# Kernel optimization log

Hardware: AMD Instinct MI355X
Metric: run time of the kernel (lower is better)

## Reference

```python
import jax, jax.numpy as jnp
import numpy as np

B, T, E, H = 2, 2048, 1024, 16
S = E // H
LN_EPS = 1e-5


def _layer_norm(x, w, b):
    # normalize over last axis (head dim s)
    mu = jnp.mean(x, axis=-1, keepdims=True)
    var = jnp.mean(jnp.square(x - mu), axis=-1, keepdims=True)
    return (x - mu) * jax.lax.rsqrt(var + LN_EPS) * w + b


def setup_inputs() -> dict:
    key = jax.random.key(0)
    ks = jax.random.split(key, 7)
    scale = 0.02
    return {
        "queries": jax.random.normal(ks[0], (B, T, E), dtype=jnp.float32),
        "keys": jax.random.normal(ks[1], (B, T, E), dtype=jnp.float32),
        "values": jax.random.normal(ks[2], (B, T, E), dtype=jnp.float32),
        "Wq": jax.random.normal(ks[3], (E, E), dtype=jnp.float32) * scale,
        "Wk": jax.random.normal(ks[4], (E, E), dtype=jnp.float32) * scale,
        "Wv": jax.random.normal(ks[5], (E, E), dtype=jnp.float32) * scale,
        "Wo": jax.random.normal(ks[6], (E, E), dtype=jnp.float32) * scale,
        "bo": jnp.zeros((E,), dtype=jnp.float32),
        "q_ln_w": jnp.ones((S,), dtype=jnp.float32),
        "q_ln_b": jnp.zeros((S,), dtype=jnp.float32),
        "k_ln_w": jnp.ones((S,), dtype=jnp.float32),
        "k_ln_b": jnp.zeros((S,), dtype=jnp.float32),
    }


def reference(queries, keys, values, Wq, Wk, Wv, Wo, bo, q_ln_w, q_ln_b, k_ln_w, k_ln_b):
    b, tq, e = queries.shape
    tk = keys.shape[1]
    h, s = H, S

    q = (queries @ Wq).reshape(b, tq, h, s)
    k = (keys @ Wk).reshape(b, tk, h, s)
    v = (values @ Wv).reshape(b, tk, h, s)

    # kqnorm: per-head LayerNorm over s
    q = _layer_norm(q, q_ln_w, q_ln_b)
    k = _layer_norm(k, k_ln_w, k_ln_b)

    # NOTE: original scales q and k each by emb**(-1/4) (NOT head_dim)
    inv4 = jnp.asarray(e, q.dtype) ** -0.25
    q = q * inv4
    k = k * inv4

    dot = jnp.einsum("bqhs,bkhs->bhqk", q, k)  # [b,h,tq,tk]

    # causal mask (mask_diagonal=False -> keep diagonal): mask j > i
    causal = jnp.tril(jnp.ones((tq, tk), dtype=bool))
    dot = jnp.where(causal, dot, jnp.asarray(-jnp.inf, dot.dtype))

    attn = jax.nn.softmax(dot, axis=-1)

    out = jnp.einsum("bhqk,bkhs->bqhs", attn, v).reshape(b, tq, e)
    return out @ Wo + bo
```

## Files before the change

kernel.cpp:

```cpp
#include <hip/hip_runtime.h>

#define Tdim 2048
#define Edim 1024
#define Hdim 16
#define Sdim 64
#define Mdim 4096
#define LN_EPS 1e-5f
#define QKSCALE 0.21233045007200477f

typedef __bf16 bf16x8 __attribute__((ext_vector_type(8)));
typedef float f32x4 __attribute__((ext_vector_type(4)));

__device__ __forceinline__ unsigned short f2bf(float f) {
  union { float f; unsigned int u; } c; c.f = f;
  unsigned int u = c.u;
  return (unsigned short)((u + 0x7FFFu + ((u >> 16) & 1u)) >> 16);
}

__device__ __forceinline__ float exp2fast(float x) {
  float r;
  asm("v_exp_f32 %0, %1" : "=v"(r) : "v"(x));
  return r;
}

__device__ __forceinline__ void gl_lds16(const void* g, void* l) {
  __builtin_amdgcn_global_load_lds(
      (const __attribute__((address_space(1))) void*)g,
      (__attribute__((address_space(3))) void*)l, 16, 0, 0);
}

__device__ __forceinline__ unsigned int pk2bf(unsigned int lo, unsigned int hi) {
  return __builtin_amdgcn_perm(hi, lo, 0x07060302u);
}

__global__ __launch_bounds__(256) void prep_k(
    const float* __restrict__ X0, const float* __restrict__ X1, const float* __restrict__ X2,
    unsigned short* __restrict__ Y0, unsigned short* __restrict__ Y1,
    unsigned short* __restrict__ Y2,
    const float* __restrict__ W0, const float* __restrict__ W1,
    const float* __restrict__ W2, const float* __restrict__ W3,
    unsigned short* __restrict__ O0, unsigned short* __restrict__ O1,
    unsigned short* __restrict__ O2, unsigned short* __restrict__ O3) {
  int bid = blockIdx.x, tid = threadIdx.x;
  if (bid < 6144) {
    int zi = bid >> 11, blk = bid & 2047;
    const float* X = zi == 0 ? X0 : zi == 1 ? X1 : X2;
    unsigned short* Y = zi == 0 ? Y0 : zi == 1 ? Y1 : Y2;
    size_t i = ((size_t)blk * 256 + tid) * 8;
    uint4 a = *(const uint4*)&X[i];
    uint4 b = *(const uint4*)&X[i + 4];
    uint4 o;
    o.x = pk2bf(a.x, a.y);
    o.y = pk2bf(a.z, a.w);
    o.z = pk2bf(b.x, b.y);
    o.w = pk2bf(b.z, b.w);
    *(uint4*)&Y[i] = o;
  } else {
    int wb = bid - 6144;
    int zi = wb >> 10, tile = wb & 1023;
    const float* W = zi == 0 ? W0 : zi == 1 ? W1 : zi == 2 ? W2 : W3;
    unsigned short* O = zi == 0 ? O0 : zi == 1 ? O1 : zi == 2 ? O2 : O3;
    __shared__ float t[32][33];
    int n0 = (tile & 31) * 32, k0 = (tile >> 5) * 32;
    int tx = tid & 31, ty = tid >> 5;
    for (int yy = ty; yy < 32; yy += 8)
      t[yy][tx] = W[(size_t)(k0 + yy) * Edim + n0 + tx];
    __syncthreads();
    for (int yy = ty; yy < 32; yy += 8)
      O[(size_t)(n0 + yy) * Edim + k0 + tx] = f2bf(t[tx][yy]);
  }
}

__global__ __launch_bounds__(256, 4) void qkv_k(
    const unsigned short* __restrict__ Qa, const unsigned short* __restrict__ Ka,
    const unsigned short* __restrict__ Va,
    const unsigned short* __restrict__ Bq, const unsigned short* __restrict__ Bk,
    const unsigned short* __restrict__ Bv,
    const float* __restrict__ qlnw, const float* __restrict__ qlnb,
    const float* __restrict__ klnw, const float* __restrict__ klnb,
    unsigned short* __restrict__ Oq, unsigned short* __restrict__ Ok,
    unsigned short* __restrict__ Ov) {
  __shared__ unsigned short As[128 * 32];
  __shared__ unsigned short Bs[128 * 32];
  int f = blockIdx.x;
  int L = (f & 7) * 96 + (f >> 3);
  int bx = L & 7, by = (L >> 3) & 31, z = L >> 8;
  const unsigned short* A = z == 0 ? Qa : z == 1 ? Ka : Va;
  const unsigned short* Bt = z == 0 ? Bq : z == 1 ? Bk : Bv;
  const float* lnw = z == 0 ? qlnw : klnw;
  const float* lnb = z == 0 ? qlnb : klnb;
  unsigned short* obf = z == 0 ? Oq : z == 1 ? Ok : Ov;

  int tid = threadIdx.x, lane = tid & 63, w = tid >> 6;
  int wr = w >> 1, wc = w & 1;
  int lg = lane >> 4, l15 = lane & 15;
  int cr = lane >> 2, sl = lane & 3;
  int m0 = by * 128, n0 = bx * 128;

  f32x4 acc[4][4];
#pragma unroll
  for (int i = 0; i < 4; ++i)
#pragma unroll
    for (int j = 0; j < 4; ++j) acc[i][j] = f32x4{0.f, 0.f, 0.f, 0.f};

  for (int ks = 0; ks < 32; ++ks) {
    int k0 = ks * 32;
    __syncthreads();
#pragma unroll
    for (int q = 0; q < 2; ++q) {
      int c = w * 2 + q, r = c * 16 + cr;
      gl_lds16(&A[(size_t)(m0 + r) * Edim + k0 + ((sl ^ (r & 3)) * 8)], &As[c * 512]);
    }
#pragma unroll
    for (int q = 0; q < 2; ++q) {
      int c = w * 2 + q, r = c * 16 + cr;
      gl_lds16(&Bt[(size_t)(n0 + r) * Edim + k0 + ((sl ^ (r & 3)) * 8)], &Bs[c * 512]);
    }
    __syncthreads();
    const unsigned short* pA = (z == 2) ? &Bs[0] : &As[0];
    const unsigned short* pB = (z == 2) ? &As[0] : &Bs[0];
    bf16x8 a[4], bb[4];
#pragma unroll
    for (int i = 0; i < 4; ++i) {
      int r = wr * 64 + i * 16 + l15;
      a[i] = *(const bf16x8*)&pA[r * 32 + ((lg ^ (r & 3)) * 8)];
    }
#pragma unroll
    for (int j = 0; j < 4; ++j) {
      int r = wc * 64 + j * 16 + l15;
      bb[j] = *(const bf16x8*)&pB[r * 32 + ((lg ^ (r & 3)) * 8)];
    }
    __builtin_amdgcn_s_setprio(1);
#pragma unroll
    for (int i = 0; i < 4; ++i)
#pragma unroll
      for (int j = 0; j < 4; ++j)
        acc[i][j] = __builtin_amdgcn_mfma_f32_16x16x32_bf16(a[i], bb[j], acc[i][j], 0, 0, 0);
    __builtin_amdgcn_s_setprio(0);
  }

  if (z < 2) {
    int mb = m0 + wr * 64;
    int h = (n0 >> 6) + wc;
#pragma unroll
    for (int i = 0; i < 4; ++i) {
#pragma unroll
      for (int r = 0; r < 4; ++r) {
        float xv[4];
#pragma unroll
        for (int j = 0; j < 4; ++j) xv[j] = acc[i][j][r];
        float sum = xv[0] + xv[1] + xv[2] + xv[3];
        float sq = xv[0] * xv[0] + xv[1] * xv[1] + xv[2] * xv[2] + xv[3] * xv[3];
#pragma unroll
        for (int off = 1; off < 16; off <<= 1) {
          sum += __shfl_xor(sum, off);
          sq += __shfl_xor(sq, off);
        }
        float mean = sum * (1.f / 64.f);
        float var = sq * (1.f / 64.f) - mean * mean;
        float rstd = rsqrtf(var + LN_EPS);
        int m = mb + i * 16 + (lg << 2) + r;
        int bb2 = m >> 11, tt = m & 2047;
        size_t base = ((size_t)(bb2 * Hdim + h) * Tdim + tt) * Sdim;
#pragma unroll
        for (int j = 0; j < 4; ++j) {
          int s = j * 16 + l15;
          float ov = ((xv[j] - mean) * rstd * lnw[s] + lnb[s]) * QKSCALE;
          obf[base + s] = f2bf(ov);
        }
      }
    }
  } else {
#pragma unroll
    for (int i = 0; i < 4; ++i)
#pragma unroll
      for (int r = 0; r < 4; ++r) {
        int hc = n0 + wr * 64 + i * 16 + (lg << 2) + r;
        int h = hc >> 6, s = hc & 63;
#pragma unroll
        for (int j = 0; j < 4; ++j) {
          int tk = m0 + wc * 64 + j * 16 + l15;
          int bb2 = tk >> 11, tt = tk & 2047;
          obf[(((size_t)(bb2 * Hdim + h) * Sdim + s)) * Tdim + tt] = f2bf(acc[i][j][r]);
        }
      }
  }
}

__global__ __launch_bounds__(256, 4) void gemmo_k(
    const unsigned short* __restrict__ A, const unsigned short* __restrict__ Bt,
    const float* __restrict__ bias, float* __restrict__ ofp) {
  __shared__ unsigned short As[128 * 32];
  __shared__ unsigned short Bs[64 * 32];
  int f = blockIdx.x;
  int L = (f & 7) * 64 + (f >> 3);
  int bx = L & 15, by = L >> 4;
  int tid = threadIdx.x, lane = tid & 63, w = tid >> 6;
  int wr = w >> 1, wc = w & 1;
  int lg = lane >> 4, l15 = lane & 15;
  int cr = lane >> 2, sl = lane & 3;
  int m0 = by * 128, n0 = bx * 64;

  f32x4 acc[4][2];
#pragma unroll
  for (int i = 0; i < 4; ++i)
#pragma unroll
    for (int j = 0; j < 2; ++j) acc[i][j] = f32x4{0.f, 0.f, 0.f, 0.f};

  for (int ks = 0; ks < 32; ++ks) {
    int k0 = ks * 32;
    __syncthreads();
#pragma unroll
    for (int q = 0; q < 2; ++q) {
      int c = w * 2 + q, r = c * 16 + cr;
      gl_lds16(&A[(size_t)(m0 + r) * Edim + k0 + ((sl ^ (r & 3)) * 8)], &As[c * 512]);
    }
    {
      int c = w, r = c * 16 + cr;
      gl_lds16(&Bt[(size_t)(n0 + r) * Edim + k0 + ((sl ^ (r & 3)) * 8)], &Bs[c * 512]);
    }
    __syncthreads();
    bf16x8 a[4], bb[2];
#pragma unroll
    for (int i = 0; i < 4; ++i) {
      int r = wr * 64 + i * 16 + l15;
      a[i] = *(const bf16x8*)&As[r * 32 + ((lg ^ (r & 3)) * 8)];
    }
#pragma unroll
    for (int j = 0; j < 2; ++j) {
      int r = wc * 32 + j * 16 + l15;
      bb[j] = *(const bf16x8*)&Bs[r * 32 + ((lg ^ (r & 3)) * 8)];
    }
    __builtin_amdgcn_s_setprio(1);
#pragma unroll
    for (int i = 0; i < 4; ++i)
#pragma unroll
      for (int j = 0; j < 2; ++j)
        acc[i][j] = __builtin_amdgcn_mfma_f32_16x16x32_bf16(a[i], bb[j], acc[i][j], 0, 0, 0);
    __builtin_amdgcn_s_setprio(0);
  }

  int mb = m0 + wr * 64, nb = n0 + wc * 32;
#pragma unroll
  for (int i = 0; i < 4; ++i)
#pragma unroll
    for (int r = 0; r < 4; ++r) {
      int m = mb + i * 16 + (lg << 2) + r;
#pragma unroll
      for (int j = 0; j < 2; ++j) {
        int n = nb + j * 16 + l15;
        ofp[(size_t)m * Edim + n] = acc[i][j][r] + bias[n];
      }
    }
}

__global__ __launch_bounds__(256) void flash_k(
    const unsigned short* __restrict__ Qn, const unsigned short* __restrict__ Kn,
    const unsigned short* __restrict__ Vb, unsigned short* __restrict__ Ob) {
  __shared__ unsigned short Qs[4096];
  __shared__ unsigned short Ks[2][4096];
  __shared__ unsigned short Vt[2][4096];
  __shared__ unsigned short Ps[4][1024];

  int wid0 = blockIdx.x;
  int idx = wid0 >> 3;
  int bh = (wid0 & 7) * 4 + (idx & 3);
  int qseg = 31 - (idx >> 2);
  int nt = qseg + 1;

  int tid = threadIdx.x, lane = tid & 63, w = tid >> 6;
  int lg = lane >> 4, l15 = lane & 15;
  int lr = lane >> 3, ls = lane & 7;
  const unsigned short* Qg = Qn + ((size_t)bh * Tdim + (size_t)qseg * 64) * Sdim;
  const unsigned short* Kg = Kn + (size_t)bh * Tdim * Sdim;
  const unsigned short* Vg = Vb + (size_t)bh * Sdim * Tdim;
  int b = bh >> 4, h = bh & 15;

  auto stageK = [&](int tt, int kb) {
    const unsigned short* src = Kg + (size_t)tt * 64 * 64;
#pragma unroll
    for (int q = 0; q < 2; ++q) {
      int c = w * 2 + q, r = c * 8 + lr;
      gl_lds16(&src[r * 64 + ((ls ^ (r & 7)) * 8)], &Ks[kb][c * 512]);
    }
  };
  auto stageV = [&](int tt, int vb) {
    const unsigned short* src = Vg + tt * 64;
#pragma unroll
    for (int q = 0; q < 2; ++q) {
      int c = w * 2 + q, r = c * 8 + lr;
      gl_lds16(&src[(size_t)r * Tdim + ((ls ^ (r & 7)) * 8)], &Vt[vb][c * 512]);
    }
  };

#pragma unroll
  for (int q = 0; q < 2; ++q) {
    int c = w * 2 + q, r = c * 8 + lr;
    gl_lds16(&Qg[r * 64 + ((ls ^ (r & 7)) * 8)], &Qs[c * 512]);
  }
  stageK(0, 0);
  stageV(0, 0);

  float mrun = -1e30f;
  float lrun[4] = {0.f, 0.f, 0.f, 0.f};
  f32x4 o[4];
#pragma unroll
  for (int js = 0; js < 4; ++js) o[js] = f32x4{0.f, 0.f, 0.f, 0.f};

  __syncthreads();

  bf16x8 aq[2];
  {
    int rq = w * 16 + l15;
    aq[0] = *(const bf16x8*)&Qs[rq * 64 + ((lg ^ (rq & 7)) * 8)];
    aq[1] = *(const bf16x8*)&Qs[rq * 64 + (((4 + lg) ^ (rq & 7)) * 8)];
  }

  for (int t = 0; t < nt; ++t) {
    int cur = t & 1;
    if (t + 1 < nt) {
      stageK(t + 1, cur ^ 1);
      stageV(t + 1, cur ^ 1);
    }
    f32x4 sf[4];
#pragma unroll
    for (int j = 0; j < 4; ++j) sf[j] = f32x4{0.f, 0.f, 0.f, 0.f};
    const unsigned short* Kc = &Ks[cur][0];
    __builtin_amdgcn_s_setprio(1);
#pragma unroll
    for (int kx = 0; kx < 2; ++kx) {
#pragma unroll
      for (int j = 0; j < 4; ++j) {
        int rk = j * 16 + l15;
        bf16x8 bk = *(const bf16x8*)&Kc[rk * 64 + (((kx * 4 + lg) ^ (rk & 7)) * 8)];
        sf[j] = __builtin_amdgcn_mfma_f32_16x16x32_bf16(aq[kx], bk, sf[j], 0, 0, 0);
      }
    }
    __builtin_amdgcn_s_setprio(0);
    if (t == qseg) {
#pragma unroll
      for (int j = 0; j < 4; ++j)
#pragma unroll
        for (int rr = 0; rr < 4; ++rr)
          if (j * 16 + l15 > w * 16 + (lg << 2) + rr) sf[j][rr] = -1e30f;
    }
    float mx = -3e38f;
#pragma unroll
    for (int j = 0; j < 4; ++j)
#pragma unroll
      for (int rr = 0; rr < 4; ++rr) mx = fmaxf(mx, sf[j][rr]);
#pragma unroll
    for (int off = 1; off < 16; off <<= 1) mx = fmaxf(mx, __shfl_xor(mx, off));
    if (__any(mx > mrun + 8.f)) {
      float mnew = fmaxf(mrun, mx);
      float alpha = exp2fast(mrun - mnew);
      mrun = mnew;
#pragma unroll
      for (int rr = 0; rr < 4; ++rr) lrun[rr] *= alpha;
#pragma unroll
      for (int js = 0; js < 4; ++js) o[js] *= alpha;
    }
    unsigned short* Pw = &Ps[w][0];
#pragma unroll
    for (int j = 0; j < 4; ++j) {
      int og = 2 * j + (l15 >> 3);
#pragma unroll
      for (int rr = 0; rr < 4; ++rr) {
        float p = exp2fast(sf[j][rr] - mrun);
        lrun[rr] += p;
        union { float f; unsigned int u; } cu;
        cu.f = p;
        int qr = (lg << 2) + rr;
        Pw[qr * 64 + ((og ^ (qr & 7)) * 8) + (l15 & 7)] = (unsigned short)(cu.u >> 16);
      }
    }
    const unsigned short* Vc = &Vt[cur][0];
    __builtin_amdgcn_s_setprio(1);
#pragma unroll
    for (int kx = 0; kx < 2; ++kx) {
      bf16x8 ap = *(const bf16x8*)&Pw[l15 * 64 + (((kx * 4 + lg) ^ (l15 & 7)) * 8)];
#pragma unroll
      for (int js = 0; js < 4; ++js) {
        int rv = js * 16 + l15;
        bf16x8 bv = *(const bf16x8*)&Vc[rv * 64 + (((kx * 4 + lg) ^ (rv & 7)) * 8)];
        o[js] = __builtin_amdgcn_mfma_f32_16x16x32_bf16(ap, bv, o[js], 0, 0, 0);
      }
    }
    __builtin_amdgcn_s_setprio(0);
    __syncthreads();
  }

#pragma unroll
  for (int rr = 0; rr < 4; ++rr) {
    float l = lrun[rr];
#pragma unroll
    for (int off = 1; off < 16; off <<= 1) l += __shfl_xor(l, off);
    float inv = 1.f / l;
    int tg = qseg * 64 + w * 16 + (lg << 2) + rr;
    size_t base = ((size_t)b * Tdim + tg) * Edim + h * 64;
#pragma unroll
    for (int js = 0; js < 4; ++js) Ob[base + js * 16 + l15] = f2bf(o[js][rr] * inv);
  }
}

extern "C" void kernel_launch(void* const* d_in, const int* in_sizes, int n_in,
                              void* d_out, int out_size, void* d_ws, size_t ws_size,
                              hipStream_t stream) {
  const float* queries = (const float*)d_in[0];
  const float* keys    = (const float*)d_in[1];
  const float* values  = (const float*)d_in[2];
  const float* Wq = (const float*)d_in[3];
  const float* Wk = (const float*)d_in[4];
  const float* Wv = (const float*)d_in[5];
  const float* Wo = (const float*)d_in[6];
  const float* bo = (const float*)d_in[7];
  const float* qlnw = (const float*)d_in[8];
  const float* qlnb = (const float*)d_in[9];
  const float* klnw = (const float*)d_in[10];
  const float* klnb = (const float*)d_in[11];
  float* out = (float*)d_out;

  unsigned short* Wtq = (unsigned short*)d_ws;
  unsigned short* Wtk = Wtq + 1024 * 1024;
  unsigned short* Wtv = Wtk + 1024 * 1024;
  unsigned short* Wto = Wtv + 1024 * 1024;
  unsigned short* Qn  = Wto + 1024 * 1024;
  unsigned short* Kn  = Qn + (size_t)Mdim * Edim;
  unsigned short* Vb  = Kn + (size_t)Mdim * Edim;
  unsigned short* Qa  = Vb + (size_t)Mdim * Edim;
  unsigned short* Ka  = Qa + (size_t)Mdim * Edim;
  unsigned short* Va  = Ka + (size_t)Mdim * Edim;
  unsigned short* Ob  = Qa;

  prep_k<<<10240, 256, 0, stream>>>(queries, keys, values, Qa, Ka, Va,
                                    Wq, Wk, Wv, Wo, Wtq, Wtk, Wtv, Wto);
  qkv_k<<<768, 256, 0, stream>>>(Qa, Ka, Va, Wtq, Wtk, Wtv,
                                 qlnw, qlnb, klnw, klnb, Qn, Kn, Vb);
  flash_k<<<1024, 256, 0, stream>>>(Qn, Kn, Vb, Ob);
  gemmo_k<<<512, 256, 0, stream>>>(Ob, Wto, bo, out);
}
```

Before: 220.7 us.

## Transpose QK^T MFMA so each lane owns one query row in softmax

Swaps the MFMA operands for the score tile so the result is S^T, with each lane's 16 values belonging to a single query row. Row max and row sum now need only two cross-lane shuffles instead of four per reduction, and P is packed two-at-a-time into bf16 and written with 8-byte LDS stores instead of 16 scalar 2-byte stores. Rescaling O and the final normalization need per-row alpha and 1/l broadcast by shuffle, which adds a few shuffles on the rare rescale path and in the epilogue.

```diff
diff --git a/kernel.cpp b/kernel.cpp
--- a/kernel.cpp
+++ b/kernel.cpp
@@ -302,7 +302,7 @@
   stageV(0, 0);
 
   float mrun = -1e30f;
-  float lrun[4] = {0.f, 0.f, 0.f, 0.f};
+  float lrun = 0.f;
   f32x4 o[4];
 #pragma unroll
   for (int js = 0; js < 4; ++js) o[js] = f32x4{0.f, 0.f, 0.f, 0.f};
@@ -315,6 +315,7 @@
     aq[0] = *(const bf16x8*)&Qs[rq * 64 + ((lg ^ (rq & 7)) * 8)];
     aq[1] = *(const bf16x8*)&Qs[rq * 64 + (((4 + lg) ^ (rq & 7)) * 8)];
   }
+  unsigned int swz = (unsigned)(l15 & 7) << 4;
 
   for (int t = 0; t < nt; ++t) {
     int cur = t & 1;
@@ -332,8 +333,8 @@
 #pragma unroll
       for (int j = 0; j < 4; ++j) {
         int rk = j * 16 + l15;
-        bf16x8 bk = *(const bf16x8*)&Kc[rk * 64 + (((kx * 4 + lg) ^ (rk & 7)) * 8)];
-        sf[j] = __builtin_amdgcn_mfma_f32_16x16x32_bf16(aq[kx], bk, sf[j], 0, 0, 0);
+        bf16x8 ak = *(const bf16x8*)&Kc[rk * 64 + (((kx * 4 + lg) ^ (rk & 7)) * 8)];
+        sf[j] = __builtin_amdgcn_mfma_f32_16x16x32_bf16(ak, aq[kx], sf[j], 0, 0, 0);
       }
     }
     __builtin_amdgcn_s_setprio(0);
@@ -342,43 +343,47 @@
       for (int j = 0; j < 4; ++j)
 #pragma unroll
         for (int rr = 0; rr < 4; ++rr)
-          if (j * 16 + l15 > w * 16 + (lg << 2) + rr) sf[j][rr] = -1e30f;
-    }
-    float mx = -3e38f;
-#pragma unroll
-    for (int j = 0; j < 4; ++j)
-#pragma unroll
-      for (int rr = 0; rr < 4; ++rr) mx = fmaxf(mx, sf[j][rr]);
-#pragma unroll
-    for (int off = 1; off < 16; off <<= 1) mx = fmaxf(mx, __shfl_xor(mx, off));
+          if (j * 16 + (lg << 2) + rr > w * 16 + l15) sf[j][rr] = -1e30f;
+    }
+    float mx = fmaxf(fmaxf(fmaxf(sf[0][0], sf[0][1]), fmaxf(sf[0][2], sf[0][3])),
+                     fmaxf(fmaxf(sf[1][0], sf[1][1]), fmaxf(sf[1][2], sf[1][3])));
+    mx = fmaxf(mx, fmaxf(fmaxf(fmaxf(sf[2][0], sf[2][1]), fmaxf(sf[2][2], sf[2][3])),
+                         fmaxf(fmaxf(sf[3][0], sf[3][1]), fmaxf(sf[3][2], sf[3][3]))));
+    mx = fmaxf(mx, __shfl_xor(mx, 16));
+    mx = fmaxf(mx, __shfl_xor(mx, 32));
     if (__any(mx > mrun + 8.f)) {
       float mnew = fmaxf(mrun, mx);
       float alpha = exp2fast(mrun - mnew);
       mrun = mnew;
-#pragma unroll
-      for (int rr = 0; rr < 4; ++rr) lrun[rr] *= alpha;
-#pragma unroll
-      for (int js = 0; js < 4; ++js) o[js] *= alpha;
+      lrun *= alpha;
+      float ar[4];
+#pragma unroll
+      for (int rr = 0; rr < 4; ++rr)
+        ar[rr] = __shfl(alpha, (lg << 4) | ((lg << 2) + rr));
+#pragma unroll
+      for (int js = 0; js < 4; ++js)
+#pragma unroll
+        for (int rr = 0; rr < 4; ++rr) o[js][rr] *= ar[rr];
     }
     unsigned short* Pw = &Ps[w][0];
 #pragma unroll
     for (int j = 0; j < 4; ++j) {
-      int og = 2 * j + (l15 >> 3);
-#pragma unroll
-      for (int rr = 0; rr < 4; ++rr) {
-        float p = exp2fast(sf[j][rr] - mrun);
-        lrun[rr] += p;
-        union { float f; unsigned int u; } cu;
-        cu.f = p;
-        int qr = (lg << 2) + rr;
-        Pw[qr * 64 + ((og ^ (qr & 7)) * 8) + (l15 & 7)] = (unsigned short)(cu.u >> 16);
-      }
+      float p0 = exp2fast(sf[j][0] - mrun);
+      float p1 = exp2fast(sf[j][1] - mrun);
+      float p2 = exp2fast(sf[j][2] - mrun);
+      float p3 = exp2fast(sf[j][3] - mrun);
+      lrun += (p0 + p1) + (p2 + p3);
+      union { float f; unsigned int u; } c0{p0}, c1{p1}, c2{p2}, c3{p3};
+      uint2 wv;
+      wv.x = pk2bf(c0.u, c1.u);
+      wv.y = pk2bf(c2.u, c3.u);
+      *(uint2*)((char*)Pw + l15 * 128 + ((j * 32 + lg * 8) ^ swz)) = wv;
     }
     const unsigned short* Vc = &Vt[cur][0];
     __builtin_amdgcn_s_setprio(1);
 #pragma unroll
     for (int kx = 0; kx < 2; ++kx) {
-      bf16x8 ap = *(const bf16x8*)&Pw[l15 * 64 + (((kx * 4 + lg) ^ (l15 & 7)) * 8)];
+      bf16x8 ap = *(const bf16x8*)((char*)Pw + l15 * 128 + ((kx * 64 + lg * 16) ^ swz));
 #pragma unroll
       for (int js = 0; js < 4; ++js) {
         int rv = js * 16 + l15;
@@ -390,16 +395,17 @@
     __syncthreads();
   }
 
+  float l = lrun;
+  l += __shfl_xor(l, 16);
+  l += __shfl_xor(l, 32);
+  float inv = 1.f / l;
 #pragma unroll
   for (int rr = 0; rr < 4; ++rr) {
-    float l = lrun[rr];
-#pragma unroll
-    for (int off = 1; off < 16; off <<= 1) l += __shfl_xor(l, off);
-    float inv = 1.f / l;
+    float invr = __shfl(inv, (lg << 4) | ((lg << 2) + rr));
     int tg = qseg * 64 + w * 16 + (lg << 2) + rr;
     size_t base = ((size_t)b * Tdim + tg) * Edim + h * 64;
 #pragma unroll
-    for (int js = 0; js < 4; ++js) Ob[base + js * 16 + l15] = f2bf(o[js][rr] * inv);
+    for (int js = 0; js < 4; ++js) Ob[base + js * 16 + l15] = f2bf(o[js][rr] * invr);
   }
 }
 
```

Measured after the change: 213.3 us. -3.4%, faster.
